# Kernel optimization log

Hardware: AMD Instinct MI355X
Metric: run time of the kernel (lower is better)

Reference implementation:

```python
import jax, jax.numpy as jnp
import numpy as np

B, S, HID = 2, 2048, 2816
NH, NKV, HD = 16, 8, 256
WINDOW = 1024
EPS = 1e-6
ROPE_THETA = 10000.0


def _rope_cos_sin(batch, seq, dim, theta):
    inv_freq = 1.0 / (theta ** (np.arange(0, dim, 2, dtype=np.float32) / dim))  # [dim/2]
    pos = np.arange(seq, dtype=np.float32)
    freqs = np.outer(pos, inv_freq)                 # [S, dim/2]
    emb = np.concatenate([freqs, freqs], axis=-1)   # [S, dim]
    cos = np.broadcast_to(np.cos(emb), (batch, seq, dim))
    sin = np.broadcast_to(np.sin(emb), (batch, seq, dim))
    return jnp.asarray(cos), jnp.asarray(sin)


def setup_inputs() -> dict:
    key = jax.random.key(0)
    ks = jax.random.split(key, 6)
    hidden_states = jax.random.normal(ks[0], (B, S, HID), dtype=jnp.float32)
    sc = 0.02
    Wq = jax.random.normal(ks[1], (NH * HD, HID), dtype=jnp.float32) * sc
    Wk = jax.random.normal(ks[2], (NKV * HD, HID), dtype=jnp.float32) * sc
    Wv = jax.random.normal(ks[3], (NKV * HD, HID), dtype=jnp.float32) * sc
    Wo = jax.random.normal(ks[4], (HID, NH * HD), dtype=jnp.float32) * sc
    q_norm_w = jnp.ones((HD,), dtype=jnp.float32) + 0.1 * jax.random.normal(ks[5], (HD,), dtype=jnp.float32)
    k_norm_w = jnp.ones((HD,), dtype=jnp.float32)
    cos, sin = _rope_cos_sin(B, S, HD, ROPE_THETA)
    return {"hidden_states": hidden_states, "Wq": Wq, "Wk": Wk, "Wv": Wv,
            "Wo": Wo, "q_norm_w": q_norm_w, "k_norm_w": k_norm_w,
            "cos": cos, "sin": sin}


def _rmsnorm(x, w):
    # HF Gemma4: effective weight, no +1 offset
    var = jnp.mean(jnp.square(x), axis=-1, keepdims=True)
    return x * jax.lax.rsqrt(var + EPS) * w


def _rotate_half(x):
    h = x.shape[-1] // 2
    return jnp.concatenate([-x[..., h:], x[..., :h]], axis=-1)


def reference(hidden_states, Wq, Wk, Wv, Wo, q_norm_w, k_norm_w, cos, sin):
    b, s, _ = hidden_states.shape
    q = (hidden_states @ Wq.T).reshape(b, s, NH, HD)
    k = (hidden_states @ Wk.T).reshape(b, s, NKV, HD)
    v = (hidden_states @ Wv.T).reshape(b, s, NKV, HD)
    q = _rmsnorm(q, q_norm_w)
    k = _rmsnorm(k, k_norm_w)
    v = _rmsnorm(v, jnp.ones((HD,), dtype=v.dtype))  # v_norm has no scale
    # RoPE with explicit cos/sin, unsqueeze at head dim (2)
    c = cos[:, :, None, :]
    sn = sin[:, :, None, :]
    q = q * c + _rotate_half(q) * sn
    k = k * c + _rotate_half(k) * sn
    # GQA: repeat kv heads to match query heads
    rep = NH // NKV
    k = jnp.repeat(k, rep, axis=2)  # [b,s,NH,HD]
    v = jnp.repeat(v, rep, axis=2)
    # scale=1.0 per torch_attention call (no 1/sqrt(d))
    scores = jnp.einsum('bqhd,bkhd->bhqk', q, k)
    i = jnp.arange(s)[:, None]
    j = jnp.arange(s)[None, :]
    mask = (j <= i) & (i - j < WINDOW)  # causal + sliding window
    scores = jnp.where(mask[None, None], scores, jnp.finfo(scores.dtype).min)
    attn = jax.nn.softmax(scores, axis=-1)
    out = jnp.einsum('bhqk,bkhd->bqhd', attn, v)  # [b,s,NH,HD]
    return out.reshape(b, s, NH * HD) @ Wo.T
```

## Files before the change

kernel.cpp:

```cpp
#include <hip/hip_runtime.h>
#include <math.h>

typedef unsigned short u16;
typedef __attribute__((ext_vector_type(8))) short short8;
typedef __attribute__((ext_vector_type(8))) _Float16 half8;
typedef __attribute__((ext_vector_type(4))) float floatx4;

#define NH 16
#define NKV 8
#define HD 256
#define SEQ 2048
#define BATCH 2
#define QD (NH * HD)
#define KVD (NKV * HD)
#define TOKS (BATCH * SEQ)
#define WINDOW 1024

__device__ __forceinline__ u16 f2h(float f) {
    _Float16 h = (_Float16)f;
    return __builtin_bit_cast(u16, h);
}
__device__ __forceinline__ float h2f(u16 u) {
    return (float)__builtin_bit_cast(_Float16, u);
}

__device__ __forceinline__ void gload16(const u16* g, u16* l) {
    __builtin_amdgcn_global_load_lds(
        (const __attribute__((address_space(1))) unsigned int*)g,
        (__attribute__((address_space(3))) unsigned int*)l,
        16, 0, 0);
}

__global__ __launch_bounds__(256) void f32_to_f16(const float* __restrict__ in,
                                                  u16* __restrict__ out, int n8) {
    const int i = blockIdx.x * 256 + threadIdx.x;
    if (i >= n8) return;
    const float4 a = *((const float4*)in + 2 * (size_t)i);
    const float4 b = *((const float4*)in + 2 * (size_t)i + 1);
    short8 r;
    r[0] = (short)f2h(a.x); r[1] = (short)f2h(a.y);
    r[2] = (short)f2h(a.z); r[3] = (short)f2h(a.w);
    r[4] = (short)f2h(b.x); r[5] = (short)f2h(b.y);
    r[6] = (short)f2h(b.z); r[7] = (short)f2h(b.w);
    *((short8*)out + i) = r;
}

#define GEMM_PRE()                                                            \
    __shared__ u16 As[128 * 32];                                              \
    __shared__ u16 Bs[128 * 32];                                              \
    const int tid = threadIdx.x;                                              \
    const int wave = tid >> 6, lane = tid & 63;                               \
    const int quad = lane >> 4, l16 = lane & 15;                              \
    const int bm = blockIdx.y * 128, bn = blockIdx.x * 128;                   \
    const int wm = (wave >> 1) * 64, wn = (wave & 1) * 64;                    \
    const int srow = wave * 32 + (lane >> 2);                                 \
    const int scol = (lane & 3) * 8;                                          \
    const u16* ga0 = A + (size_t)(bm + srow) * K + scol;                      \
    const u16* ga1 = ga0 + (size_t)16 * K;                                    \
    const u16* gb0 = B + (size_t)(bn + srow) * K + scol;                      \
    const u16* gb1 = gb0 + (size_t)16 * K;                                    \
    u16* lA0 = &As[wave * 1024];                                              \
    u16* lA1 = &As[wave * 1024 + 512];                                        \
    u16* lB0 = &Bs[wave * 1024];                                              \
    u16* lB1 = &Bs[wave * 1024 + 512];                                        \
    floatx4 acc[4][4];                                                        \
    _Pragma("unroll")                                                         \
    for (int i = 0; i < 4; ++i)                                               \
        _Pragma("unroll")                                                     \
        for (int j = 0; j < 4; ++j) acc[i][j] = (floatx4){0.f, 0.f, 0.f, 0.f};\
    const int kTiles = K >> 5;                                                \
    for (int kt = 0; kt < kTiles; ++kt) {                                     \
        __syncthreads();                                                      \
        gload16(ga0, lA0);                                                    \
        gload16(ga1, lA1);                                                    \
        gload16(gb0, lB0);                                                    \
        gload16(gb1, lB1);                                                    \
        ga0 += 32; ga1 += 32; gb0 += 32; gb1 += 32;                           \
        __syncthreads();                                                      \
        half8 af[4], bfr[4];                                                  \
        _Pragma("unroll")                                                     \
        for (int i = 0; i < 4; ++i)                                           \
            af[i] = *(const half8*)(&As[(wm + i * 16 + l16) * 32 + quad * 8]);\
        _Pragma("unroll")                                                     \
        for (int j = 0; j < 4; ++j)                                           \
            bfr[j] = *(const half8*)(&Bs[(wn + j * 16 + l16) * 32 + quad * 8]);\
        _Pragma("unroll")                                                     \
        for (int i = 0; i < 4; ++i)                                           \
            _Pragma("unroll")                                                 \
            for (int j = 0; j < 4; ++j)                                       \
                acc[i][j] = __builtin_amdgcn_mfma_f32_16x16x32_f16(af[i], bfr[j], acc[i][j], 0, 0, 0); \
    }

template<bool OUTF32>
__global__ __launch_bounds__(256) void gemm_lds(const u16* __restrict__ A,
                                                const u16* __restrict__ B,
                                                void* __restrict__ Cp,
                                                int M, int N, int K) {
    GEMM_PRE()
#pragma unroll
    for (int i = 0; i < 4; ++i) {
#pragma unroll
        for (int j = 0; j < 4; ++j) {
            const int row0 = bm + wm + i * 16 + quad * 4;
            const int col = bn + wn + j * 16 + l16;
#pragma unroll
            for (int r = 0; r < 4; ++r) {
                if constexpr (OUTF32)
                    ((float*)Cp)[(size_t)(row0 + r) * N + col] = acc[i][j][r];
                else
                    ((u16*)Cp)[(size_t)(row0 + r) * N + col] = f2h(acc[i][j][r]);
            }
        }
    }
}

__global__ __launch_bounds__(256) void gemm_qkv(const u16* __restrict__ A,
                                                const u16* __restrict__ B,
                                                u16* __restrict__ Qb,
                                                u16* __restrict__ Kb,
                                                u16* __restrict__ Vt,
                                                int M, int N, int K) {
    GEMM_PRE()
#pragma unroll
    for (int i = 0; i < 4; ++i) {
#pragma unroll
        for (int j = 0; j < 4; ++j) {
            const int row0 = bm + wm + i * 16 + quad * 4;
            const int col = bn + wn + j * 16 + l16;
#pragma unroll
            for (int r = 0; r < 4; ++r) {
                const u16 hv = f2h(acc[i][j][r]);
                if (bn < 4096)
                    Qb[(size_t)(row0 + r) * QD + col] = hv;
                else if (bn < 6144)
                    Kb[(size_t)(row0 + r) * KVD + (col - 4096)] = hv;
                else
                    Vt[(size_t)(col - 6144) * TOKS + row0 + r] = hv;
            }
        }
    }
}

__global__ __launch_bounds__(256) void norm_rope_kernel(
        u16* __restrict__ Q, u16* __restrict__ K,
        const float* __restrict__ qw, const float* __restrict__ kw,
        const float* __restrict__ cosp, const float* __restrict__ sinp) {
    const int w = blockIdx.x * 4 + (threadIdx.x >> 6);
    const int lane = threadIdx.x & 63;
    const int row = w >> 5;
    const int sub = w & 31;
    if (sub >= 24) return;

    u16* ptr;
    const float* wt;
    if (sub < 16) { ptr = Q + (size_t)row * QD + sub * HD;         wt = qw; }
    else          { ptr = K + (size_t)row * KVD + (sub - 16) * HD; wt = kw; }

    const int d = lane * 4;
    uint2 raw = *(const uint2*)(ptr + d);
    float x[4];
    x[0] = h2f((u16)(raw.x & 0xffffu));
    x[1] = h2f((u16)(raw.x >> 16));
    x[2] = h2f((u16)(raw.y & 0xffffu));
    x[3] = h2f((u16)(raw.y >> 16));

    float ss = x[0] * x[0] + x[1] * x[1] + x[2] * x[2] + x[3] * x[3];
#pragma unroll
    for (int m = 1; m < 64; m <<= 1) ss += __shfl_xor(ss, m, 64);
    const float sc = rsqrtf(ss * (1.0f / 256.0f) + 1e-6f);

    float nrm[4];
#pragma unroll
    for (int i = 0; i < 4; ++i) nrm[i] = x[i] * sc * wt[d + i];

    const size_t cbase = (size_t)row * HD + d;
    const float sgn = (lane < 32) ? -1.0f : 1.0f;
    float out[4];
#pragma unroll
    for (int i = 0; i < 4; ++i) {
        float pn = __shfl_xor(nrm[i], 32, 64);
        float c = cosp[cbase + i];
        float s = sinp[cbase + i];
        out[i] = nrm[i] * c + sgn * pn * s;
    }

    uint2 o;
    o.x = (unsigned int)f2h(out[0]) | ((unsigned int)f2h(out[1]) << 16);
    o.y = (unsigned int)f2h(out[2]) | ((unsigned int)f2h(out[3]) << 16);
    *(uint2*)(ptr + d) = o;
}

__global__ __launch_bounds__(256) void vnorm_kernel(u16* __restrict__ Vt) {
    const int tok = blockIdx.x * 256 + threadIdx.x;
    const int kvh = blockIdx.y;
    u16* p = Vt + (size_t)kvh * HD * TOKS + tok;
    float ss = 0.f;
#pragma unroll 4
    for (int d = 0; d < HD; ++d) {
        float v = h2f(p[(size_t)d * TOKS]);
        ss += v * v;
    }
    const float sc = rsqrtf(ss * (1.0f / 256.0f) + 1e-6f);
#pragma unroll 4
    for (int d = 0; d < HD; ++d) {
        const size_t idx = (size_t)d * TOKS;
        p[idx] = f2h(h2f(p[idx]) * sc);
    }
}

#define QBLK 64
#define KVBLK 64

__global__ __launch_bounds__(256, 2) void attn_mfma(
        const u16* __restrict__ Q, const u16* __restrict__ K,
        const u16* __restrict__ Vt, u16* __restrict__ O) {
    __shared__ u16 Ks[64 * 256];
    __shared__ u16 Vs[256 * 64];
    __shared__ u16 Ps[4][16 * 72];

    const int tid = threadIdx.x;
    const int wave = tid >> 6, lane = tid & 63;
    const int quad = lane >> 4, l16 = lane & 15;
    const int q0 = blockIdx.x * QBLK;
    const int h = blockIdx.y, b = blockIdx.z;
    const int kvh = h >> 1;

    half8 qf[8];
    {
        const u16* qp = Q + (size_t)(b * SEQ + q0 + wave * 16 + l16) * QD + h * HD + quad * 8;
#pragma unroll
        for (int s = 0; s < 8; ++s) qf[s] = *(const half8*)(qp + s * 32);
    }

    float mrow[4], lrow[4];
#pragma unroll
    for (int r = 0; r < 4; ++r) { mrow[r] = -1e30f; lrow[r] = 0.f; }
    floatx4 o[16];
#pragma unroll
    for (int n = 0; n < 16; ++n) o[n] = (floatx4){0.f, 0.f, 0.f, 0.f};

    int lo = q0 - (WINDOW - 1);
    const int t0 = (lo > 0 ? lo : 0) >> 6;
    const int tq = q0 >> 6;

    const int kr2 = wave * 2 + (lane >> 5);
    const int kcb = (lane & 31) * 16;
    const int vr8 = wave * 8 + (lane >> 3);
    const int vcb = (lane & 7) * 16;

    for (int t = t0; t <= tq; ++t) {
        const int k0 = t * KVBLK;
        __syncthreads();
#pragma unroll
        for (int p = 0; p < 8; ++p) {
            const int row = p * 8 + kr2;
            const int scb = kcb ^ ((row & 7) << 4);
            const u16* g = K + (size_t)(b * SEQ + k0 + row) * KVD + kvh * HD + (scb >> 1);
            gload16(g, &Ks[p * 2048 + wave * 512]);
        }
#pragma unroll
        for (int p = 0; p < 8; ++p) {
            const int row = p * 32 + vr8;
            const int scb = vcb ^ ((row & 7) << 4);
            const u16* g = Vt + (size_t)(kvh * HD + row) * TOKS + b * SEQ + k0 + (scb >> 1);
            gload16(g, &Vs[p * 2048 + wave * 512]);
        }
        __syncthreads();

        floatx4 sf[4];
#pragma unroll
        for (int j = 0; j < 4; ++j) sf[j] = (floatx4){0.f, 0.f, 0.f, 0.f};
        __builtin_amdgcn_s_setprio(1);
#pragma unroll
        for (int s = 0; s < 8; ++s) {
#pragma unroll
            for (int j = 0; j < 4; ++j) {
                half8 bf = *(const half8*)(&Ks[(j * 16 + l16) * 256 +
                                               ((s * 32 + quad * 8) ^ ((l16 & 7) << 3))]);
                sf[j] = __builtin_amdgcn_mfma_f32_16x16x32_f16(qf[s], bf, sf[j], 0, 0, 0);
            }
        }
        __builtin_amdgcn_s_setprio(0);

        const bool needMask = (t == tq) || ((q0 + QBLK - 1) - k0 >= WINDOW);
        if (needMask) {
#pragma unroll
            for (int j = 0; j < 4; ++j) {
                const int kg = k0 + j * 16 + l16;
#pragma unroll
                for (int r = 0; r < 4; ++r) {
                    const int qg = q0 + wave * 16 + quad * 4 + r;
                    if (kg > qg || qg - kg >= WINDOW) sf[j][r] = -1e30f;
                }
            }
        }

#pragma unroll
        for (int r = 0; r < 4; ++r) {
            float mx = fmaxf(fmaxf(sf[0][r], sf[1][r]), fmaxf(sf[2][r], sf[3][r]));
            mx = fmaxf(mx, __shfl_xor(mx, 1, 64));
            mx = fmaxf(mx, __shfl_xor(mx, 2, 64));
            mx = fmaxf(mx, __shfl_xor(mx, 4, 64));
            mx = fmaxf(mx, __shfl_xor(mx, 8, 64));
            const float mnew = fmaxf(mrow[r], mx);
            const float rescale = __expf(mrow[r] - mnew);
            mrow[r] = mnew;
            float pv[4], ssum = 0.f;
#pragma unroll
            for (int j = 0; j < 4; ++j) {
                pv[j] = __expf(sf[j][r] - mnew);
                ssum += pv[j];
            }
            ssum += __shfl_xor(ssum, 1, 64);
            ssum += __shfl_xor(ssum, 2, 64);
            ssum += __shfl_xor(ssum, 4, 64);
            ssum += __shfl_xor(ssum, 8, 64);
            lrow[r] = lrow[r] * rescale + ssum;
#pragma unroll
            for (int n = 0; n < 16; ++n) o[n][r] *= rescale;
#pragma unroll
            for (int j = 0; j < 4; ++j)
                Ps[wave][(quad * 4 + r) * 72 + j * 16 + l16] = f2h(pv[j]);
        }

        __builtin_amdgcn_s_setprio(1);
#pragma unroll
        for (int s2 = 0; s2 < 2; ++s2) {
            half8 pa = *(const half8*)(&Ps[wave][l16 * 72 + s2 * 32 + quad * 8]);
#pragma unroll
            for (int n = 0; n < 16; ++n) {
                half8 vb = *(const half8*)(&Vs[(n * 16 + l16) * 64 +
                                               ((s2 * 32 + quad * 8) ^ ((l16 & 7) << 3))]);
                o[n] = __builtin_amdgcn_mfma_f32_16x16x32_f16(pa, vb, o[n], 0, 0, 0);
            }
        }
        __builtin_amdgcn_s_setprio(0);
    }

#pragma unroll
    for (int r = 0; r < 4; ++r) {
        const float inv = 1.0f / lrow[r];
        const size_t base = (size_t)(b * SEQ + q0 + wave * 16 + quad * 4 + r) * QD + h * HD + l16;
#pragma unroll
        for (int n = 0; n < 16; ++n)
            O[base + n * 16] = f2h(o[n][r] * inv);
    }
}

extern "C" void kernel_launch(void* const* d_in, const int* in_sizes, int n_in,
                              void* d_out, int out_size, void* d_ws, size_t ws_size,
                              hipStream_t stream) {
    const float* X    = (const float*)d_in[0];
    const float* Wq   = (const float*)d_in[1];
    const float* Wk   = (const float*)d_in[2];
    const float* Wv   = (const float*)d_in[3];
    const float* Wo   = (const float*)d_in[4];
    const float* qw   = (const float*)d_in[5];
    const float* kw   = (const float*)d_in[6];
    const float* cosp = (const float*)d_in[7];
    const float* sinp = (const float*)d_in[8];

    char* ws = (char*)d_ws;
    u16* Qb  = (u16*)(ws);
    u16* Kb  = (u16*)(ws + (size_t)33554432);
    u16* Vt  = (u16*)(ws + (size_t)50331648);
    u16* Xh  = (u16*)(ws + (size_t)67108864);
    u16* Ob  = (u16*)(ws + (size_t)67108864);
    u16* Woh = (u16*)(ws);

    u16* Wqkv = (u16*)d_out;

    const dim3 blk(256);
    f32_to_f16<<<dim3(5632), blk, 0, stream>>>(X,  Xh, 11534336 / 8);
    f32_to_f16<<<dim3(5632), blk, 0, stream>>>(Wq, Wqkv, 11534336 / 8);
    f32_to_f16<<<dim3(2816), blk, 0, stream>>>(Wk, Wqkv + (size_t)4096 * 2816, 5767168 / 8);
    f32_to_f16<<<dim3(2816), blk, 0, stream>>>(Wv, Wqkv + (size_t)6144 * 2816, 5767168 / 8);
    gemm_qkv<<<dim3(8192 / 128, 4096 / 128), blk, 0, stream>>>(Xh, Wqkv, Qb, Kb, Vt, 4096, 8192, 2816);
    norm_rope_kernel<<<dim3((BATCH * SEQ * 32) / 4), blk, 0, stream>>>(Qb, Kb, qw, kw, cosp, sinp);
    vnorm_kernel<<<dim3(TOKS / 256, NKV), blk, 0, stream>>>(Vt);
    attn_mfma<<<dim3(SEQ / QBLK, NH, BATCH), blk, 0, stream>>>(Qb, Kb, Vt, Ob);
    f32_to_f16<<<dim3(5632), blk, 0, stream>>>(Wo, Woh, 11534336 / 8);
    gemm_lds<true><<<dim3(2816 / 128, 4096 / 128), blk, 0, stream>>>(Ob, Woh, d_out, 4096, 2816, 4096);
}
```

Before: 833.3 us.

## Rewrite GEMMs with double-buffered LDS, swizzle, 256x128 tiles and grid remap

Replaces both the QKV and output projection GEMMs with a single templated kernel. It uses 512-thread blocks with 256x128 tiles, double-buffered LDS, and prefetches the next K tile before computing the current one, waiting on vmcnt. It also XOR-swizzles LDS columns to avoid bank conflicts and remaps the 1D grid so that concurrently scheduled blocks share operand rows in cache. The goal is to hide global load latency and remove the two-barrier serial load/compute pattern. The cost is more LDS per block and more complex synchronization.

```diff
diff --git a/kernel.cpp b/kernel.cpp
--- a/kernel.cpp
+++ b/kernel.cpp
@@ -45,97 +45,102 @@
     *((short8*)out + i) = r;
 }
 
-#define GEMM_PRE()                                                            \
-    __shared__ u16 As[128 * 32];                                              \
-    __shared__ u16 Bs[128 * 32];                                              \
-    const int tid = threadIdx.x;                                              \
-    const int wave = tid >> 6, lane = tid & 63;                               \
-    const int quad = lane >> 4, l16 = lane & 15;                              \
-    const int bm = blockIdx.y * 128, bn = blockIdx.x * 128;                   \
-    const int wm = (wave >> 1) * 64, wn = (wave & 1) * 64;                    \
-    const int srow = wave * 32 + (lane >> 2);                                 \
-    const int scol = (lane & 3) * 8;                                          \
-    const u16* ga0 = A + (size_t)(bm + srow) * K + scol;                      \
-    const u16* ga1 = ga0 + (size_t)16 * K;                                    \
-    const u16* gb0 = B + (size_t)(bn + srow) * K + scol;                      \
-    const u16* gb1 = gb0 + (size_t)16 * K;                                    \
-    u16* lA0 = &As[wave * 1024];                                              \
-    u16* lA1 = &As[wave * 1024 + 512];                                        \
-    u16* lB0 = &Bs[wave * 1024];                                              \
-    u16* lB1 = &Bs[wave * 1024 + 512];                                        \
-    floatx4 acc[4][4];                                                        \
-    _Pragma("unroll")                                                         \
-    for (int i = 0; i < 4; ++i)                                               \
-        _Pragma("unroll")                                                     \
-        for (int j = 0; j < 4; ++j) acc[i][j] = (floatx4){0.f, 0.f, 0.f, 0.f};\
-    const int kTiles = K >> 5;                                                \
-    for (int kt = 0; kt < kTiles; ++kt) {                                     \
-        __syncthreads();                                                      \
-        gload16(ga0, lA0);                                                    \
-        gload16(ga1, lA1);                                                    \
-        gload16(gb0, lB0);                                                    \
-        gload16(gb1, lB1);                                                    \
-        ga0 += 32; ga1 += 32; gb0 += 32; gb1 += 32;                           \
-        __syncthreads();                                                      \
-        half8 af[4], bfr[4];                                                  \
-        _Pragma("unroll")                                                     \
-        for (int i = 0; i < 4; ++i)                                           \
-            af[i] = *(const half8*)(&As[(wm + i * 16 + l16) * 32 + quad * 8]);\
-        _Pragma("unroll")                                                     \
-        for (int j = 0; j < 4; ++j)                                           \
-            bfr[j] = *(const half8*)(&Bs[(wn + j * 16 + l16) * 32 + quad * 8]);\
-        _Pragma("unroll")                                                     \
-        for (int i = 0; i < 4; ++i)                                           \
-            _Pragma("unroll")                                                 \
-            for (int j = 0; j < 4; ++j)                                       \
-                acc[i][j] = __builtin_amdgcn_mfma_f32_16x16x32_f16(af[i], bfr[j], acc[i][j], 0, 0, 0); \
-    }
-
-template<bool OUTF32>
-__global__ __launch_bounds__(256) void gemm_lds(const u16* __restrict__ A,
-                                                const u16* __restrict__ B,
-                                                void* __restrict__ Cp,
-                                                int M, int N, int K) {
-    GEMM_PRE()
+template<int MODE>
+__global__ __launch_bounds__(512, 4) void gemm_db(
+        const u16* __restrict__ A, const u16* __restrict__ B,
+        void* __restrict__ Cq, void* __restrict__ Ck, void* __restrict__ Cv,
+        int N, int K, int ntn) {
+    __shared__ u16 As[2 * 8192];
+    __shared__ u16 Bs[2 * 4096];
+
+    const int tid = threadIdx.x;
+    const int wave = tid >> 6, lane = tid & 63;
+    const int quad = lane >> 4, l16 = lane & 15;
+    const int wr = wave >> 1, wc = wave & 1;
+
+    const int nwg = (int)gridDim.x;
+    const int wg0 = (int)blockIdx.x;
+    const int wg = (wg0 & 7) * (nwg >> 3) + (wg0 >> 3);
+    const int bm = (wg / ntn) * 256;
+    const int bn = (wg % ntn) * 128;
+
+    const int lrow = lane >> 2;
+    const int lcol = (((lane & 3) ^ ((lane >> 3) & 3)) << 3);
+    const u16* gA  = A + (size_t)(bm + wave * 32 + lrow) * K + lcol;
+    const u16* gA2 = gA + (size_t)16 * K;
+    const u16* gB  = B + (size_t)(bn + wave * 16 + lrow) * K + lcol;
+
+    floatx4 acc[4][4];
+#pragma unroll
+    for (int i = 0; i < 4; ++i)
+#pragma unroll
+        for (int j = 0; j < 4; ++j) acc[i][j] = (floatx4){0.f, 0.f, 0.f, 0.f};
+
+#define STG(tt, bb)                                                           \
+    {                                                                         \
+        const int ko_ = (tt) << 5;                                            \
+        gload16(gA + ko_,  &As[(bb) * 8192 + wave * 1024]);                   \
+        gload16(gA2 + ko_, &As[(bb) * 8192 + wave * 1024 + 512]);             \
+        gload16(gB + ko_,  &Bs[(bb) * 4096 + wave * 512]);                    \
+    }
+
+    STG(0, 0);
+
+    const int rdsw = ((quad ^ ((l16 >> 1) & 3)) << 3);
+    const int aoff = (wr * 64 + l16) * 32 + rdsw;
+    const int boff = (wc * 64 + l16) * 32 + rdsw;
+
+    const int NT = K >> 5;
+    for (int t = 0; t < NT; ++t) {
+        const int cb = t & 1;
+        if (t + 1 < NT) {
+            STG(t + 1, cb ^ 1);
+            asm volatile("s_waitcnt vmcnt(3)" ::: "memory");
+        } else {
+            asm volatile("s_waitcnt vmcnt(0)" ::: "memory");
+        }
+        __builtin_amdgcn_sched_barrier(0);
+        __builtin_amdgcn_s_barrier();
+        __builtin_amdgcn_sched_barrier(0);
+
+        half8 aq[4], bq[4];
+#pragma unroll
+        for (int i = 0; i < 4; ++i)
+            aq[i] = *(const half8*)(&As[cb * 8192 + aoff + i * 512]);
+#pragma unroll
+        for (int j = 0; j < 4; ++j)
+            bq[j] = *(const half8*)(&Bs[cb * 4096 + boff + j * 512]);
+#pragma unroll
+        for (int i = 0; i < 4; ++i)
+#pragma unroll
+            for (int j = 0; j < 4; ++j)
+                acc[i][j] = __builtin_amdgcn_mfma_f32_16x16x32_f16(aq[i], bq[j], acc[i][j], 0, 0, 0);
+
+        __builtin_amdgcn_sched_barrier(0);
+        __builtin_amdgcn_s_barrier();
+        __builtin_amdgcn_sched_barrier(0);
+    }
+#undef STG
+
 #pragma unroll
     for (int i = 0; i < 4; ++i) {
 #pragma unroll
         for (int j = 0; j < 4; ++j) {
-            const int row0 = bm + wm + i * 16 + quad * 4;
-            const int col = bn + wn + j * 16 + l16;
+            const int row0 = bm + wr * 64 + i * 16 + quad * 4;
+            const int col = bn + wc * 64 + j * 16 + l16;
 #pragma unroll
             for (int r = 0; r < 4; ++r) {
-                if constexpr (OUTF32)
-                    ((float*)Cp)[(size_t)(row0 + r) * N + col] = acc[i][j][r];
-                else
-                    ((u16*)Cp)[(size_t)(row0 + r) * N + col] = f2h(acc[i][j][r]);
-            }
-        }
-    }
-}
-
-__global__ __launch_bounds__(256) void gemm_qkv(const u16* __restrict__ A,
-                                                const u16* __restrict__ B,
-                                                u16* __restrict__ Qb,
-                                                u16* __restrict__ Kb,
-                                                u16* __restrict__ Vt,
-                                                int M, int N, int K) {
-    GEMM_PRE()
-#pragma unroll
-    for (int i = 0; i < 4; ++i) {
-#pragma unroll
-        for (int j = 0; j < 4; ++j) {
-            const int row0 = bm + wm + i * 16 + quad * 4;
-            const int col = bn + wn + j * 16 + l16;
-#pragma unroll
-            for (int r = 0; r < 4; ++r) {
-                const u16 hv = f2h(acc[i][j][r]);
-                if (bn < 4096)
-                    Qb[(size_t)(row0 + r) * QD + col] = hv;
-                else if (bn < 6144)
-                    Kb[(size_t)(row0 + r) * KVD + (col - 4096)] = hv;
-                else
-                    Vt[(size_t)(col - 6144) * TOKS + row0 + r] = hv;
+                if constexpr (MODE == 1) {
+                    ((float*)Cq)[(size_t)(row0 + r) * N + col] = acc[i][j][r];
+                } else {
+                    const u16 hv = f2h(acc[i][j][r]);
+                    if (bn < 4096)
+                        ((u16*)Cq)[(size_t)(row0 + r) * QD + col] = hv;
+                    else if (bn < 6144)
+                        ((u16*)Ck)[(size_t)(row0 + r) * KVD + (col - 4096)] = hv;
+                    else
+                        ((u16*)Cv)[(size_t)(col - 6144) * TOKS + row0 + r] = hv;
+                }
             }
         }
     }
@@ -375,10 +380,10 @@
     f32_to_f16<<<dim3(5632), blk, 0, stream>>>(Wq, Wqkv, 11534336 / 8);
     f32_to_f16<<<dim3(2816), blk, 0, stream>>>(Wk, Wqkv + (size_t)4096 * 2816, 5767168 / 8);
     f32_to_f16<<<dim3(2816), blk, 0, stream>>>(Wv, Wqkv + (size_t)6144 * 2816, 5767168 / 8);
-    gemm_qkv<<<dim3(8192 / 128, 4096 / 128), blk, 0, stream>>>(Xh, Wqkv, Qb, Kb, Vt, 4096, 8192, 2816);
+    gemm_db<0><<<dim3(1024), dim3(512), 0, stream>>>(Xh, Wqkv, Qb, Kb, Vt, 8192, 2816, 64);
     norm_rope_kernel<<<dim3((BATCH * SEQ * 32) / 4), blk, 0, stream>>>(Qb, Kb, qw, kw, cosp, sinp);
     vnorm_kernel<<<dim3(TOKS / 256, NKV), blk, 0, stream>>>(Vt);
     attn_mfma<<<dim3(SEQ / QBLK, NH, BATCH), blk, 0, stream>>>(Qb, Kb, Vt, Ob);
     f32_to_f16<<<dim3(5632), blk, 0, stream>>>(Wo, Woh, 11534336 / 8);
-    gemm_lds<true><<<dim3(2816 / 128, 4096 / 128), blk, 0, stream>>>(Ob, Woh, d_out, 4096, 2816, 4096);
-}
+    gemm_db<1><<<dim3(352), dim3(512), 0, stream>>>(Ob, Woh, d_out, nullptr, nullptr, 2816, 4096, 22);
+}
```

New measurement: 731.9 us. 12.2% less time.
